# Performance work log

Hardware: AMD Instinct MI355X
Metric: run time of the kernel (lower is better)

The kernel has to match this reference:

```python
import jax, jax.numpy as jnp
import numpy as np

D_MODEL = 1024
N_HEADS = 16
HEAD_DIM = D_MODEL // N_HEADS
D_FF = 4096
BATCH = 4
SEQ = 2048
EPS = 1e-6


def setup_inputs() -> dict:
    key = jax.random.key(0)
    ks = jax.random.split(key, 12)
    s = 0.02
    return {
        "x": jax.random.normal(ks[0], (BATCH, SEQ, D_MODEL), dtype=jnp.float32),
        "rope_cos": jax.random.uniform(ks[1], (SEQ, HEAD_DIM), dtype=jnp.float32),
        "rope_sin": jax.random.uniform(ks[2], (SEQ, HEAD_DIM), dtype=jnp.float32),
        "g1": jnp.ones((D_MODEL,), jnp.float32),
        "g2": jnp.ones((D_MODEL,), jnp.float32),
        "wq": jax.random.normal(ks[3], (D_MODEL, D_MODEL), dtype=jnp.float32) * s,
        "wk": jax.random.normal(ks[4], (D_MODEL, D_MODEL), dtype=jnp.float32) * s,
        "wv": jax.random.normal(ks[5], (D_MODEL, D_MODEL), dtype=jnp.float32) * s,
        "wo": jax.random.normal(ks[6], (D_MODEL, D_MODEL), dtype=jnp.float32) * s,
        "w_gate": jax.random.normal(ks[7], (D_MODEL, D_FF), dtype=jnp.float32) * s,
        "w_up": jax.random.normal(ks[8], (D_MODEL, D_FF), dtype=jnp.float32) * s,
        "w_down": jax.random.normal(ks[9], (D_FF, D_MODEL), dtype=jnp.float32) * s,
    }


def _rmsnorm(x, g):
    var = jnp.mean(x * x, axis=-1, keepdims=True)
    return x * jax.lax.rsqrt(var + EPS) * g


def _rotate_half(x):
    x1, x2 = jnp.split(x, 2, axis=-1)
    return jnp.concatenate([-x2, x1], axis=-1)


def _apply_rope(x, cos, sin):
    # x: [B,H,S,D]; cos/sin: [S,D] broadcast to [1,1,S,D]
    return x * cos[None, None] + _rotate_half(x) * sin[None, None]


def _block(x, rope_cos, rope_sin, g1, g2, wq, wk, wv, wo, w_gate, w_up, w_down):
    B, S, _ = x.shape
    # --- manual causal attention with RoPE ---
    xn = _rmsnorm(x, g1)
    def heads(w):
        return (xn @ w).reshape(B, S, N_HEADS, HEAD_DIM).transpose(0, 2, 1, 3)
    q = _apply_rope(heads(wq), rope_cos, rope_sin)
    k = _apply_rope(heads(wk), rope_cos, rope_sin)
    v = heads(wv)
    scores = jnp.einsum('bhqd,bhkd->bhqk', q, k) / jnp.sqrt(jnp.float32(HEAD_DIM))
    causal = jnp.tril(jnp.ones((S, S), dtype=bool))
    scores = jnp.where(causal[None, None], scores, jnp.finfo(scores.dtype).min)
    attn = jax.nn.softmax(scores, axis=-1)
    ctx = jnp.einsum('bhqk,bhkd->bhqd', attn, v)
    ctx = ctx.transpose(0, 2, 1, 3).reshape(B, S, D_MODEL)
    x = x + ctx @ wo
    # --- SwiGLU MLP ---
    xn2 = _rmsnorm(x, g2)
    h = jax.nn.silu(xn2 @ w_gate) * (xn2 @ w_up)
    return x + h @ w_down


def reference(x, rope_cos, rope_sin, g1, g2, wq, wk, wv, wo, w_gate, w_up, w_down):
    return _block(x, rope_cos, rope_sin, g1, g2, wq, wk, wv, wo, w_gate, w_up, w_down)
```

## Files before the change

### kernel.cpp

```cpp
#include <hip/hip_runtime.h>
#include <cstdint>
#include <cstddef>

#define D_MODEL 1024
#define NH 16
#define HD 64
#define DFF 4096
#define BATCH 4
#define SEQ 2048
#define NROWS (BATCH*SEQ)
#define QKVW 3072

typedef uint16_t u16;
typedef __attribute__((ext_vector_type(8))) __bf16 bf16x8;
typedef __attribute__((ext_vector_type(4))) float f32x4;
typedef __attribute__((ext_vector_type(8))) u16 u16x8;
typedef __attribute__((ext_vector_type(4))) u16 u16x4;

__device__ __forceinline__ u16 f2bf(float x){
  union { float f; uint32_t u; } v; v.f = x;
  uint32_t r = v.u + 0x7fffu + ((v.u >> 16) & 1u);
  return (u16)(r >> 16);
}
__device__ __forceinline__ float bf2f(u16 h){
  union { uint32_t u; float f; } v; v.u = ((uint32_t)h) << 16; return v.f;
}
__device__ __forceinline__ void gload16(const void* g, void* l){
  __builtin_amdgcn_global_load_lds(
      (const __attribute__((address_space(1))) void*)g,
      (__attribute__((address_space(3))) void*)l, 16, 0, 0);
}
__device__ __forceinline__ const bf16x8* swzp(const u16* base, int row, int chunk){
  return (const bf16x8*)((const char*)base + row*128 + (((chunk ^ (row & 7)) << 4)));
}

__global__ __launch_bounds__(256) void k_transpose_w(const float* __restrict__ W,
                                                     u16* __restrict__ WT, int K, int N){
  __shared__ float tile[64][68];
  const int n0 = blockIdx.x*64, k0 = blockIdx.y*64;
  const int t = threadIdx.x;
  const int rr = t >> 4, cc = t & 15;
  #pragma unroll
  for (int i = 0; i < 4; ++i){
    int row = i*16 + rr;
    float4 v = *(const float4*)(W + (size_t)(k0+row)*N + n0 + cc*4);
    tile[row][cc*4+0] = v.x; tile[row][cc*4+1] = v.y;
    tile[row][cc*4+2] = v.z; tile[row][cc*4+3] = v.w;
  }
  __syncthreads();
  #pragma unroll
  for (int i = 0; i < 4; ++i){
    int nrow = i*16 + rr;
    int kc = cc*4;
    u16x4 o;
    o[0] = f2bf(tile[kc+0][nrow]);
    o[1] = f2bf(tile[kc+1][nrow]);
    o[2] = f2bf(tile[kc+2][nrow]);
    o[3] = f2bf(tile[kc+3][nrow]);
    *(u16x4*)(WT + (size_t)(n0+nrow)*K + k0 + kc) = o;
  }
}

__global__ __launch_bounds__(256) void k_rmsnorm(const float* __restrict__ x,
                                                 const float* __restrict__ g,
                                                 u16* __restrict__ out){
  const int row = blockIdx.x; const int t = threadIdx.x;
  const float* xr = x + (size_t)row*D_MODEL;
  float4 v = *(const float4*)(xr + t*4);
  float ss = v.x*v.x + v.y*v.y + v.z*v.z + v.w*v.w;
  #pragma unroll
  for (int off = 1; off < 64; off <<= 1) ss += __shfl_xor(ss, off);
  __shared__ float wsum[4];
  if ((t & 63) == 0) wsum[t>>6] = ss;
  __syncthreads();
  float tot = wsum[0]+wsum[1]+wsum[2]+wsum[3];
  float sc = rsqrtf(tot * (1.0f/(float)D_MODEL) + 1e-6f);
  float4 gg = *(const float4*)(g + t*4);
  u16x4 o;
  o[0]=f2bf(v.x*sc*gg.x); o[1]=f2bf(v.y*sc*gg.y);
  o[2]=f2bf(v.z*sc*gg.z); o[3]=f2bf(v.w*sc*gg.w);
  *(u16x4*)(out + (size_t)row*D_MODEL + t*4) = o;
}

template<int NREP, int MODE>
__global__ __launch_bounds__(512, 2) void k_gemm8(
    const u16* __restrict__ A, const u16* __restrict__ BT,
    u16* __restrict__ Cb, float* __restrict__ Cf,
    const float* __restrict__ resid, const u16* __restrict__ gate,
    int M, int N, int K, int nbx)
{
  __shared__ __align__(16) u16 lA[2][16384];
  __shared__ __align__(16) u16 lB[2][NREP*4096];
  const int t = threadIdx.x, wid = t >> 6, lane = t & 63, lr = lane & 15, lg = lane >> 4;
  const int wr = wid >> 2, wc = wid & 3;
  const int nwg = gridDim.x, bid = blockIdx.x;
  const int wg = (bid & 7) * (nwg >> 3) + (bid >> 3);
  const int bx = wg % nbx, by = wg / nbx;
  const int m0 = by * 256, n0 = bx * (NREP * 64);
  const int NT = K >> 6;

  f32x4 acc[8][NREP];
  #pragma unroll
  for (int i=0;i<8;++i)
    #pragma unroll
    for (int j=0;j<NREP;++j) acc[i][j] = (f32x4){0.f,0.f,0.f,0.f};

  #define STAGE_A(kt,p) { \
    _Pragma("unroll") \
    for (int i=0;i<4;++i){ \
      int ci = i*512 + t; int row = ci>>3, c = ci&7; \
      gload16(A + (size_t)(m0+row)*K + (kt)*64 + ((c ^ (row&7))*8), \
              (char*)lA[p] + i*8192 + wid*1024); } }
  #define STAGE_B(kt,p) { \
    _Pragma("unroll") \
    for (int i=0;i<NREP;++i){ \
      int ci = i*512 + t; int row = ci>>3, c = ci&7; \
      gload16(BT + (size_t)(n0+row)*K + (kt)*64 + ((c ^ (row&7))*8), \
              (char*)lB[p] + i*8192 + wid*1024); } }
  #define WAIT_L() { if constexpr (NREP==4) asm volatile("s_waitcnt vmcnt(8)" ::: "memory"); \
                     else                   asm volatile("s_waitcnt vmcnt(6)" ::: "memory"); }

  STAGE_A(0,0); STAGE_B(0,0);
  STAGE_A(1,1); STAGE_B(1,1);
  WAIT_L();
  __builtin_amdgcn_sched_barrier(0);
  __builtin_amdgcn_s_barrier();
  __builtin_amdgcn_sched_barrier(0);

  for (int kt = 0; kt < NT; ++kt){
    const int p = kt & 1;
    const u16* a = lA[p];
    const u16* b = lB[p];
    bf16x8 af[8][2], bfr[NREP][2];
    #pragma unroll
    for (int mi=0;mi<4;++mi){
      int row = wr*128 + mi*16 + lr;
      af[mi][0] = *swzp(a, row,   lg);
      af[mi][1] = *swzp(a, row, 4+lg);
    }
    #pragma unroll
    for (int ni=0;ni<NREP/2;++ni){
      int row = wc*(NREP*16) + ni*16 + lr;
      bfr[ni][0] = *swzp(b, row,   lg);
      bfr[ni][1] = *swzp(b, row, 4+lg);
    }
    __builtin_amdgcn_s_setprio(1);
    #pragma unroll
    for (int mi=0;mi<4;++mi)
      #pragma unroll
      for (int ni=0;ni<NREP/2;++ni){
        acc[mi][ni] = __builtin_amdgcn_mfma_f32_16x16x32_bf16(af[mi][0], bfr[ni][0], acc[mi][ni], 0,0,0);
        acc[mi][ni] = __builtin_amdgcn_mfma_f32_16x16x32_bf16(af[mi][1], bfr[ni][1], acc[mi][ni], 0,0,0);
      }
    __builtin_amdgcn_s_setprio(0);
    #pragma unroll
    for (int mi=4;mi<8;++mi){
      int row = wr*128 + mi*16 + lr;
      af[mi][0] = *swzp(a, row,   lg);
      af[mi][1] = *swzp(a, row, 4+lg);
    }
    #pragma unroll
    for (int ni=NREP/2;ni<NREP;++ni){
      int row = wc*(NREP*16) + ni*16 + lr;
      bfr[ni][0] = *swzp(b, row,   lg);
      bfr[ni][1] = *swzp(b, row, 4+lg);
    }
    __builtin_amdgcn_s_setprio(1);
    #pragma unroll
    for (int mi=4;mi<8;++mi)
      #pragma unroll
      for (int ni=0;ni<NREP/2;++ni){
        acc[mi][ni] = __builtin_amdgcn_mfma_f32_16x16x32_bf16(af[mi][0], bfr[ni][0], acc[mi][ni], 0,0,0);
        acc[mi][ni] = __builtin_amdgcn_mfma_f32_16x16x32_bf16(af[mi][1], bfr[ni][1], acc[mi][ni], 0,0,0);
      }
    __builtin_amdgcn_s_setprio(0);
    asm volatile("s_waitcnt lgkmcnt(0)" ::: "memory");
    __builtin_amdgcn_sched_barrier(0);
    __builtin_amdgcn_s_barrier();
    __builtin_amdgcn_sched_barrier(0);
    if (kt + 2 < NT) STAGE_A(kt+2, p);
    __builtin_amdgcn_s_setprio(1);
    #pragma unroll
    for (int mi=0;mi<4;++mi)
      #pragma unroll
      for (int ni=NREP/2;ni<NREP;++ni){
        acc[mi][ni] = __builtin_amdgcn_mfma_f32_16x16x32_bf16(af[mi][0], bfr[ni][0], acc[mi][ni], 0,0,0);
        acc[mi][ni] = __builtin_amdgcn_mfma_f32_16x16x32_bf16(af[mi][1], bfr[ni][1], acc[mi][ni], 0,0,0);
      }
    __builtin_amdgcn_s_setprio(0);
    if (kt + 2 < NT) STAGE_B(kt+2, p);
    __builtin_amdgcn_s_setprio(1);
    #pragma unroll
    for (int mi=4;mi<8;++mi)
      #pragma unroll
      for (int ni=NREP/2;ni<NREP;++ni){
        acc[mi][ni] = __builtin_amdgcn_mfma_f32_16x16x32_bf16(af[mi][0], bfr[ni][0], acc[mi][ni], 0,0,0);
        acc[mi][ni] = __builtin_amdgcn_mfma_f32_16x16x32_bf16(af[mi][1], bfr[ni][1], acc[mi][ni], 0,0,0);
      }
    __builtin_amdgcn_s_setprio(0);
    __builtin_amdgcn_sched_barrier(0);
    if (kt + 2 < NT) { WAIT_L(); }
    else             { asm volatile("s_waitcnt vmcnt(0)" ::: "memory"); }
    __builtin_amdgcn_s_barrier();
    __builtin_amdgcn_sched_barrier(0);
  }

  #pragma unroll
  for (int mi=0;mi<8;++mi)
    #pragma unroll
    for (int ni=0;ni<NREP;++ni){
      int mbase = m0 + wr*128 + mi*16 + lg*4;
      int n = n0 + wc*(NREP*16) + ni*16 + lr;
      #pragma unroll
      for (int r=0;r<4;++r){
        size_t idx = (size_t)(mbase + r)*N + n;
        float vv = acc[mi][ni][r];
        if (MODE == 0) Cb[idx] = f2bf(vv);
        else if (MODE == 1) Cf[idx] = resid[idx] + vv;
        else { float gt = bf2f(gate[idx]); float sg = gt / (1.f + __expf(-gt)); Cb[idx] = f2bf(sg * vv); }
      }
    }
  #undef STAGE_A
  #undef STAGE_B
  #undef WAIT_L
}

__global__ __launch_bounds__(256) void k_rope(u16* __restrict__ qkv,
                                              const float* __restrict__ cs,
                                              const float* __restrict__ sn){
  int tid = blockIdx.x*256 + threadIdx.x;
  int d = tid & 31, h = (tid >> 5) & 15, s = (tid >> 9) & 2047, b = tid >> 20;
  size_t base = ((size_t)(b*SEQ + s))*QKVW + h*HD;
  float c1 = cs[s*HD + d],      s1 = sn[s*HD + d];
  float c2 = cs[s*HD + d + 32], s2 = sn[s*HD + d + 32];
  float q1 = bf2f(qkv[base+d]), q2 = bf2f(qkv[base+d+32]);
  qkv[base+d]    = f2bf(q1*c1 - q2*s1);
  qkv[base+d+32] = f2bf(q2*c2 + q1*s2);
  size_t kb = base + 1024;
  float k1 = bf2f(qkv[kb+d]), k2 = bf2f(qkv[kb+d+32]);
  qkv[kb+d]    = f2bf(k1*c1 - k2*s1);
  qkv[kb+d+32] = f2bf(k2*c2 + k1*s2);
}

__global__ __launch_bounds__(256) void k_transpose_v(const u16* __restrict__ qkv,
                                                     u16* __restrict__ vt){
  const int s0 = blockIdx.x*64; const int bh = blockIdx.y;
  const int b = bh >> 4, h = bh & 15;
  __shared__ u16 tile[64][72];
  const int t = threadIdx.x;
  #pragma unroll
  for (int i=0;i<2;++i){
    int c = i*256 + t;
    int sr = c >> 3, ch = c & 7;
    u16x8 vv = *(const u16x8*)(qkv + (size_t)(b*SEQ + s0 + sr)*QKVW + 2048 + h*HD + ch*8);
    #pragma unroll
    for (int j=0;j<8;++j) tile[sr][ch*8+j] = vv[j];
  }
  __syncthreads();
  #pragma unroll
  for (int i=0;i<2;++i){
    int c = i*256 + t;
    int dr = c >> 3, ch = c & 7;
    u16x8 o;
    #pragma unroll
    for (int j=0;j<8;++j) o[j] = tile[ch*8+j][dr];
    *(u16x8*)(vt + (size_t)(bh*HD + dr)*SEQ + s0 + ch*8) = o;
  }
}

__global__ __launch_bounds__(256) void k_attn(const u16* __restrict__ qkv,
                                              const u16* __restrict__ vt,
                                              u16* __restrict__ ctx){
  const int bh = blockIdx.x;
  const int qt = (int)gridDim.y - 1 - (int)blockIdx.y;
  const int b = bh >> 4, h = bh & 15;
  const int t = threadIdx.x, w = t >> 6, lane = t & 63, lr = lane & 15, lg = lane >> 4;
  __shared__ __align__(16) u16 kld[64*64];
  __shared__ __align__(16) u16 vld[64*64];
  __shared__ __align__(16) u16 pld[4][16*64];

  const int qrow = qt*64 + w*16 + lr;
  const u16* qbase = qkv + (size_t)(b*SEQ + qrow)*QKVW + h*HD;
  bf16x8 qa0 = *(const bf16x8*)(qbase + lg*8);
  bf16x8 qa1 = *(const bf16x8*)(qbase + 32 + lg*8);

  float mreg[4], lreg[4]; f32x4 o[4];
  #pragma unroll
  for (int r=0;r<4;++r){ mreg[r] = -INFINITY; lreg[r] = 0.f; }
  #pragma unroll
  for (int g=0;g<4;++g) o[g] = (f32x4){0.f,0.f,0.f,0.f};

  for (int it = 0; it <= qt; ++it){
    const int kv0 = it*64;
    __syncthreads();
    #pragma unroll
    for (int i=0;i<2;++i){
      int ci = i*256 + t;
      int row = ci >> 3, c = ci & 7, cg = c ^ (row & 7);
      gload16(qkv + (size_t)(b*SEQ + kv0 + row)*QKVW + 1024 + h*HD + cg*8,
              (char*)kld + i*4096 + w*1024);
      gload16(vt + (size_t)(bh*HD + row)*SEQ + kv0 + cg*8,
              (char*)vld + i*4096 + w*1024);
    }
    __syncthreads();

    f32x4 s[4];
    #pragma unroll
    for (int nf=0;nf<4;++nf) s[nf] = (f32x4){0.f,0.f,0.f,0.f};
    #pragma unroll
    for (int nf=0;nf<4;++nf){
      int row = nf*16 + lr;
      s[nf] = __builtin_amdgcn_mfma_f32_16x16x32_bf16(qa0, *swzp(kld,row,  lg), s[nf], 0,0,0);
      s[nf] = __builtin_amdgcn_mfma_f32_16x16x32_bf16(qa1, *swzp(kld,row,4+lg), s[nf], 0,0,0);
    }
    const bool domask = (it == qt);
    float p[4][4], rm[4];
    #pragma unroll
    for (int r=0;r<4;++r) rm[r] = -INFINITY;
    #pragma unroll
    for (int nf=0;nf<4;++nf)
      #pragma unroll
      for (int r=0;r<4;++r){
        float v = s[nf][r]*0.125f;
        if (domask && (kv0 + nf*16 + lr > qt*64 + w*16 + lg*4 + r)) v = -INFINITY;
        p[nf][r] = v; rm[r] = fmaxf(rm[r], v);
      }
    #pragma unroll
    for (int off=1; off<16; off<<=1)
      #pragma unroll
      for (int r=0;r<4;++r) rm[r] = fmaxf(rm[r], __shfl_xor(rm[r], off));
    float al[4];
    #pragma unroll
    for (int r=0;r<4;++r){
      float mn = fmaxf(mreg[r], rm[r]);
      al[r] = __expf(mreg[r] - mn);
      mreg[r] = mn;
    }
    #pragma unroll
    for (int nf=0;nf<4;++nf)
      #pragma unroll
      for (int r=0;r<4;++r) p[nf][r] = __expf(p[nf][r] - mreg[r]);
    float ps[4];
    #pragma unroll
    for (int r=0;r<4;++r) ps[r] = p[0][r]+p[1][r]+p[2][r]+p[3][r];
    #pragma unroll
    for (int off=1; off<16; off<<=1)
      #pragma unroll
      for (int r=0;r<4;++r) ps[r] += __shfl_xor(ps[r], off);
    #pragma unroll
    for (int r=0;r<4;++r) lreg[r] = lreg[r]*al[r] + ps[r];
    #pragma unroll
    for (int g=0;g<4;++g)
      #pragma unroll
      for (int r=0;r<4;++r) o[g][r] *= al[r];

    #pragma unroll
    for (int nf=0;nf<4;++nf)
      #pragma unroll
      for (int r=0;r<4;++r){
        int prow = lg*4 + r;
        int pb = ((nf*16 + lr)*2) ^ ((prow & 7) << 4);
        *(u16*)((char*)(pld[w]) + prow*128 + pb) = f2bf(p[nf][r]);
      }
    bf16x8 pa0 = *swzp(pld[w], lr,   lg);
    bf16x8 pa1 = *swzp(pld[w], lr, 4+lg);
    #pragma unroll
    for (int g=0;g<4;++g){
      o[g] = __builtin_amdgcn_mfma_f32_16x16x32_bf16(pa0, *swzp(vld, g*16+lr,   lg), o[g], 0,0,0);
      o[g] = __builtin_amdgcn_mfma_f32_16x16x32_bf16(pa1, *swzp(vld, g*16+lr, 4+lg), o[g], 0,0,0);
    }
  }
  #pragma unroll
  for (int g=0; g<4; ++g){
    int col = h*HD + g*16 + lr;
    #pragma unroll
    for (int r=0;r<4;++r){
      int row = qt*64 + w*16 + lg*4 + r;
      ctx[(size_t)(b*SEQ + row)*D_MODEL + col] = f2bf(o[g][r] / lreg[r]);
    }
  }
}

extern "C" void kernel_launch(void* const* d_in, const int* in_sizes, int n_in,
                              void* d_out, int out_size, void* d_ws, size_t ws_size,
                              hipStream_t stream){
  const float* x  = (const float*)d_in[0];
  const float* rc = (const float*)d_in[1];
  const float* rs = (const float*)d_in[2];
  const float* g1 = (const float*)d_in[3];
  const float* g2 = (const float*)d_in[4];
  const float* wq = (const float*)d_in[5];
  const float* wk = (const float*)d_in[6];
  const float* wv = (const float*)d_in[7];
  const float* wo = (const float*)d_in[8];
  const float* wg = (const float*)d_in[9];
  const float* wu = (const float*)d_in[10];
  const float* wd = (const float*)d_in[11];
  float* out = (float*)d_out;

  char* ws = (char*)d_ws;
  const size_t MB = 1024*1024;
  u16* wqkvT = (u16*)(ws + 0);
  u16* woT   = (u16*)(ws + 6*MB);
  u16* wgT   = (u16*)(ws + 8*MB);
  u16* wuT   = (u16*)(ws + 16*MB);
  u16* wdT   = (u16*)(ws + 24*MB);
  float* x1  = (float*)(ws + 32*MB);
  u16* xn    = (u16*)(ws + 64*MB);
  u16* qkv   = (u16*)(ws + 80*MB);
  u16* vtb   = (u16*)(ws + 128*MB);
  u16* gb    = (u16*)(ws + 144*MB);

  dim3 blk(256);
  k_transpose_w<<<dim3(16,16),blk,0,stream>>>(wq, wqkvT,             1024, 1024);
  k_transpose_w<<<dim3(16,16),blk,0,stream>>>(wk, wqkvT + 1024*1024, 1024, 1024);
  k_transpose_w<<<dim3(16,16),blk,0,stream>>>(wv, wqkvT + 2048*1024, 1024, 1024);
  k_transpose_w<<<dim3(16,16),blk,0,stream>>>(wo, woT, 1024, 1024);
  k_transpose_w<<<dim3(64,16),blk,0,stream>>>(wg, wgT, 1024, 4096);
  k_transpose_w<<<dim3(64,16),blk,0,stream>>>(wu, wuT, 1024, 4096);
  k_transpose_w<<<dim3(16,64),blk,0,stream>>>(wd, wdT, 4096, 1024);

  k_rmsnorm<<<dim3(NROWS),blk,0,stream>>>(x, g1, xn);

  k_gemm8<4,0><<<dim3(384),dim3(512),0,stream>>>(xn, wqkvT, qkv, nullptr, nullptr, nullptr,
                                                 NROWS, QKVW, 1024, 12);

  k_rope<<<dim3((BATCH*SEQ*NH*32)/256),blk,0,stream>>>(qkv, rc, rs);
  k_transpose_v<<<dim3(32,64),blk,0,stream>>>(qkv, vtb);
  k_attn<<<dim3(64,32),blk,0,stream>>>(qkv, vtb, xn);

  k_gemm8<2,1><<<dim3(256),dim3(512),0,stream>>>(xn, woT, nullptr, x1, x, nullptr,
                                                 NROWS, 1024, 1024, 8);

  k_rmsnorm<<<dim3(NROWS),blk,0,stream>>>(x1, g2, xn);

  k_gemm8<4,0><<<dim3(512),dim3(512),0,stream>>>(xn, wgT, gb, nullptr, nullptr, nullptr,
                                                 NROWS, 4096, 1024, 16);
  k_gemm8<4,2><<<dim3(512),dim3(512),0,stream>>>(xn, wuT, gb, nullptr, nullptr, gb,
                                                 NROWS, 4096, 1024, 16);
  k_gemm8<2,1><<<dim3(256),dim3(512),0,stream>>>(gb, wdT, nullptr, out, x1, nullptr,
                                                 NROWS, 1024, 4096, 8);
}
```

Baseline: 643.8 us.

## Double-buffer K/V tiles and transpose MFMA operands in attention kernel

The attention kernel now double-buffers K and V tiles in LDS, issuing the next tile's async loads before computing the current one, with one barrier per iteration instead of two. The QK^T and PV MFMAs swap operand order so each lane holds one query row's scores. That reduces the row-max and row-sum reductions to two cross-lane shuffles, and exp2 with a prescaled log2e replaces __expf. It doubles LDS use, which may reduce occupancy, and uses a padded P buffer instead of a swizzled one.

```diff
diff --git a/kernel.cpp b/kernel.cpp
--- a/kernel.cpp
+++ b/kernel.cpp
@@ -268,116 +268,119 @@
   }
 }
 
-__global__ __launch_bounds__(256) void k_attn(const u16* __restrict__ qkv,
-                                              const u16* __restrict__ vt,
-                                              u16* __restrict__ ctx){
+__global__ __launch_bounds__(256) void k_attn3(const u16* __restrict__ qkv,
+                                               const u16* __restrict__ vt,
+                                               u16* __restrict__ ctx){
   const int bh = blockIdx.x;
   const int qt = (int)gridDim.y - 1 - (int)blockIdx.y;
   const int b = bh >> 4, h = bh & 15;
-  const int t = threadIdx.x, w = t >> 6, lane = t & 63, lr = lane & 15, lg = lane >> 4;
-  __shared__ __align__(16) u16 kld[64*64];
-  __shared__ __align__(16) u16 vld[64*64];
-  __shared__ __align__(16) u16 pld[4][16*64];
-
-  const int qrow = qt*64 + w*16 + lr;
-  const u16* qbase = qkv + (size_t)(b*SEQ + qrow)*QKVW + h*HD;
-  bf16x8 qa0 = *(const bf16x8*)(qbase + lg*8);
-  bf16x8 qa1 = *(const bf16x8*)(qbase + 32 + lg*8);
-
-  float mreg[4], lreg[4]; f32x4 o[4];
-  #pragma unroll
-  for (int r=0;r<4;++r){ mreg[r] = -INFINITY; lreg[r] = 0.f; }
-  #pragma unroll
-  for (int g=0;g<4;++g) o[g] = (f32x4){0.f,0.f,0.f,0.f};
-
-  for (int it = 0; it <= qt; ++it){
+  const int t = threadIdx.x, wid = t >> 6, lane = t & 63;
+  const int lr = lane & 15, lg = lane >> 4;
+  __shared__ __align__(16) u16 kld[2][64*64];
+  __shared__ __align__(16) u16 vld[2][64*64];
+  __shared__ __align__(16) u16 pld[4][16][72];
+
+  const int qw0 = qt*64 + wid*16;
+  const int qg = qw0 + lr;
+  const u16* qrow = qkv + (size_t)(b*SEQ + qg)*QKVW + h*HD;
+  bf16x8 qf0 = *(const bf16x8*)(qrow + lg*8);
+  bf16x8 qf1 = *(const bf16x8*)(qrow + 32 + lg*8);
+
+  f32x4 o[4];
+  #pragma unroll
+  for (int dt=0;dt<4;++dt) o[dt] = (f32x4){0.f,0.f,0.f,0.f};
+  float m_run = -INFINITY, l_run = 0.f;
+  const float SC2 = 0.125f * 1.4426950408889634f;
+
+  const int nt = qt + 1;
+
+  #define ASTAGE(it_, p_) { \
+    const int kv0_ = (it_)*64; \
+    _Pragma("unroll") \
+    for (int i=0;i<2;++i){ \
+      int ci = i*256 + t; int row = ci>>3, c = ci&7, cg = c ^ (row&7); \
+      gload16(qkv + (size_t)(b*SEQ + kv0_ + row)*QKVW + 1024 + h*HD + cg*8, \
+              (char*)kld[p_] + i*4096 + wid*1024); \
+      gload16(vt + (size_t)(bh*HD + row)*SEQ + kv0_ + cg*8, \
+              (char*)vld[p_] + i*4096 + wid*1024); \
+    } }
+
+  ASTAGE(0, 0);
+  asm volatile("s_waitcnt vmcnt(0)" ::: "memory");
+  __builtin_amdgcn_sched_barrier(0);
+  __builtin_amdgcn_s_barrier();
+  __builtin_amdgcn_sched_barrier(0);
+
+  for (int it = 0; it < nt; ++it){
+    const int p = it & 1;
+    if (it + 1 < nt) ASTAGE(it+1, p^1);
     const int kv0 = it*64;
-    __syncthreads();
-    #pragma unroll
-    for (int i=0;i<2;++i){
-      int ci = i*256 + t;
-      int row = ci >> 3, c = ci & 7, cg = c ^ (row & 7);
-      gload16(qkv + (size_t)(b*SEQ + kv0 + row)*QKVW + 1024 + h*HD + cg*8,
-              (char*)kld + i*4096 + w*1024);
-      gload16(vt + (size_t)(bh*HD + row)*SEQ + kv0 + cg*8,
-              (char*)vld + i*4096 + w*1024);
-    }
-    __syncthreads();
-
     f32x4 s[4];
     #pragma unroll
-    for (int nf=0;nf<4;++nf) s[nf] = (f32x4){0.f,0.f,0.f,0.f};
-    #pragma unroll
-    for (int nf=0;nf<4;++nf){
-      int row = nf*16 + lr;
-      s[nf] = __builtin_amdgcn_mfma_f32_16x16x32_bf16(qa0, *swzp(kld,row,  lg), s[nf], 0,0,0);
-      s[nf] = __builtin_amdgcn_mfma_f32_16x16x32_bf16(qa1, *swzp(kld,row,4+lg), s[nf], 0,0,0);
+    for (int c=0;c<4;++c) s[c] = (f32x4){0.f,0.f,0.f,0.f};
+    #pragma unroll
+    for (int c=0;c<4;++c){
+      s[c] = __builtin_amdgcn_mfma_f32_16x16x32_bf16(*swzp(kld[p], c*16+lr,   lg), qf0, s[c], 0,0,0);
+      s[c] = __builtin_amdgcn_mfma_f32_16x16x32_bf16(*swzp(kld[p], c*16+lr, 4+lg), qf1, s[c], 0,0,0);
     }
     const bool domask = (it == qt);
-    float p[4][4], rm[4];
-    #pragma unroll
-    for (int r=0;r<4;++r) rm[r] = -INFINITY;
-    #pragma unroll
-    for (int nf=0;nf<4;++nf)
+    float pm = -INFINITY;
+    #pragma unroll
+    for (int c=0;c<4;++c)
       #pragma unroll
       for (int r=0;r<4;++r){
-        float v = s[nf][r]*0.125f;
-        if (domask && (kv0 + nf*16 + lr > qt*64 + w*16 + lg*4 + r)) v = -INFINITY;
-        p[nf][r] = v; rm[r] = fmaxf(rm[r], v);
-      }
-    #pragma unroll
-    for (int off=1; off<16; off<<=1)
-      #pragma unroll
-      for (int r=0;r<4;++r) rm[r] = fmaxf(rm[r], __shfl_xor(rm[r], off));
-    float al[4];
-    #pragma unroll
-    for (int r=0;r<4;++r){
-      float mn = fmaxf(mreg[r], rm[r]);
-      al[r] = __expf(mreg[r] - mn);
-      mreg[r] = mn;
-    }
-    #pragma unroll
-    for (int nf=0;nf<4;++nf)
-      #pragma unroll
-      for (int r=0;r<4;++r) p[nf][r] = __expf(p[nf][r] - mreg[r]);
-    float ps[4];
-    #pragma unroll
-    for (int r=0;r<4;++r) ps[r] = p[0][r]+p[1][r]+p[2][r]+p[3][r];
-    #pragma unroll
-    for (int off=1; off<16; off<<=1)
-      #pragma unroll
-      for (int r=0;r<4;++r) ps[r] += __shfl_xor(ps[r], off);
-    #pragma unroll
-    for (int r=0;r<4;++r) lreg[r] = lreg[r]*al[r] + ps[r];
-    #pragma unroll
-    for (int g=0;g<4;++g)
-      #pragma unroll
-      for (int r=0;r<4;++r) o[g][r] *= al[r];
-
-    #pragma unroll
-    for (int nf=0;nf<4;++nf)
+        float v = s[c][r]*SC2;
+        if (domask && (kv0 + c*16 + lg*4 + r > qg)) v = -INFINITY;
+        s[c][r] = v;
+        pm = fmaxf(pm, v);
+      }
+    pm = fmaxf(pm, __shfl_xor(pm, 16));
+    pm = fmaxf(pm, __shfl_xor(pm, 32));
+    float mnew = fmaxf(m_run, pm);
+    float alpha = exp2f(fmaxf(m_run - mnew, -100.f));
+    m_run = mnew;
+    float lsum = 0.f;
+    #pragma unroll
+    for (int c=0;c<4;++c)
       #pragma unroll
       for (int r=0;r<4;++r){
-        int prow = lg*4 + r;
-        int pb = ((nf*16 + lr)*2) ^ ((prow & 7) << 4);
-        *(u16*)((char*)(pld[w]) + prow*128 + pb) = f2bf(p[nf][r]);
-      }
-    bf16x8 pa0 = *swzp(pld[w], lr,   lg);
-    bf16x8 pa1 = *swzp(pld[w], lr, 4+lg);
-    #pragma unroll
-    for (int g=0;g<4;++g){
-      o[g] = __builtin_amdgcn_mfma_f32_16x16x32_bf16(pa0, *swzp(vld, g*16+lr,   lg), o[g], 0,0,0);
-      o[g] = __builtin_amdgcn_mfma_f32_16x16x32_bf16(pa1, *swzp(vld, g*16+lr, 4+lg), o[g], 0,0,0);
-    }
-  }
-  #pragma unroll
-  for (int g=0; g<4; ++g){
-    int col = h*HD + g*16 + lr;
-    #pragma unroll
-    for (int r=0;r<4;++r){
-      int row = qt*64 + w*16 + lg*4 + r;
-      ctx[(size_t)(b*SEQ + row)*D_MODEL + col] = f2bf(o[g][r] / lreg[r]);
-    }
+        s[c][r] = exp2f(s[c][r] - mnew);
+        lsum += s[c][r];
+      }
+    lsum += __shfl_xor(lsum, 16);
+    lsum += __shfl_xor(lsum, 32);
+    l_run = l_run*alpha + lsum;
+    #pragma unroll
+    for (int dt=0;dt<4;++dt)
+      #pragma unroll
+      for (int r=0;r<4;++r) o[dt][r] *= alpha;
+    #pragma unroll
+    for (int c=0;c<4;++c)
+      #pragma unroll
+      for (int r=0;r<4;++r)
+        pld[wid][lr][c*16 + lg*4 + r] = f2bf(s[c][r]);
+    bf16x8 pb0 = *(const bf16x8*)(&pld[wid][lr][lg*8]);
+    bf16x8 pb1 = *(const bf16x8*)(&pld[wid][lr][32 + lg*8]);
+    #pragma unroll
+    for (int dt=0;dt<4;++dt){
+      o[dt] = __builtin_amdgcn_mfma_f32_16x16x32_bf16(*swzp(vld[p], dt*16+lr,   lg), pb0, o[dt], 0,0,0);
+      o[dt] = __builtin_amdgcn_mfma_f32_16x16x32_bf16(*swzp(vld[p], dt*16+lr, 4+lg), pb1, o[dt], 0,0,0);
+    }
+    asm volatile("s_waitcnt vmcnt(0)" ::: "memory");
+    __builtin_amdgcn_sched_barrier(0);
+    __builtin_amdgcn_s_barrier();
+    __builtin_amdgcn_sched_barrier(0);
+  }
+  #undef ASTAGE
+
+  const float inv = 1.f / l_run;
+  u16* crow_out = ctx + (size_t)(b*SEQ + qg)*D_MODEL + h*HD;
+  #pragma unroll
+  for (int dt=0;dt<4;++dt){
+    u16x4 st;
+    #pragma unroll
+    for (int r=0;r<4;++r) st[r] = f2bf(o[dt][r] * inv);
+    *(u16x4*)(crow_out + dt*16 + lg*4) = st;
   }
 }
 
@@ -427,7 +430,7 @@
 
   k_rope<<<dim3((BATCH*SEQ*NH*32)/256),blk,0,stream>>>(qkv, rc, rs);
   k_transpose_v<<<dim3(32,64),blk,0,stream>>>(qkv, vtb);
-  k_attn<<<dim3(64,32),blk,0,stream>>>(qkv, vtb, xn);
+  k_attn3<<<dim3(64,32),blk,0,stream>>>(qkv, vtb, xn);
 
   k_gemm8<2,1><<<dim3(256),dim3(512),0,stream>>>(xn, woT, nullptr, x1, x, nullptr,
                                                  NROWS, 1024, 1024, 8);
```

After: 597.8 us. 7.1% less time.
